# Performance work log

Measured on AMD Instinct MI355X. Metric: run time of the kernel, lower is better.

The kernel has to match this reference:

```python
import jax, jax.numpy as jnp
import numpy as np


def setup_inputs() -> dict:
    key = jax.random.key(0)
    kq, kk, kv = jax.random.split(key, 3)
    B, H, L, D = 1, 16, 4096, 64
    q = jax.random.normal(kq, (B, H, L, D), dtype=jnp.float32)
    k = jax.random.normal(kk, (B, H, L, D), dtype=jnp.float32)
    v = jax.random.normal(kv, (B, H, L, D), dtype=jnp.float32)
    return {"q": q, "k": k, "v": v}


def reference(q, k, v):
    # scale = sqrt(head_dim), matching q.size(-1) ** 0.5 in the torch module
    scale = jnp.asarray(q.shape[-1], q.dtype) ** 0.5
    # [b,h,l,m] attention scores, materialized as in the original (no flash tiling)
    attn = jnp.einsum('bhlk,bhmk->bhlm', q, k) / scale
    attn = jax.nn.softmax(attn, axis=-1)
    out = jnp.einsum('bhlm,bhmk->bhlk', attn, v)
    return out
```

## Files before the change

kernel.cpp:

```cpp
#include <hip/hip_runtime.h>
#include <hip/hip_bf16.h>


#define LSEQ 4096
#define DH   64
#define NH   16
#define QBLK 256
#define KBLK 64
#define NT   (LSEQ / KBLK)

typedef float  f32x4   __attribute__((ext_vector_type(4)));
typedef short  short8v __attribute__((ext_vector_type(8)));

__device__ __forceinline__ short f2bf(float f) {
    unsigned int u = __builtin_bit_cast(unsigned int, f);
    u = (u + 0x7FFFu + ((u >> 16) & 1u)) >> 16;
    return (short)u;
}

__device__ __forceinline__ short f2bf_rz(float f) {
    return (short)(__builtin_bit_cast(unsigned int, f) >> 16);
}

__device__ __forceinline__ short8v pack8(const float4& a, const float4& b) {
    short8v f;
    f[0] = f2bf(a.x); f[1] = f2bf(a.y); f[2] = f2bf(a.z); f[3] = f2bf(a.w);
    f[4] = f2bf(b.x); f[5] = f2bf(b.y); f[6] = f2bf(b.z); f[7] = f2bf(b.w);
    return f;
}

#define SWZ(row, slot) ((((slot) ^ ((row) & 7)) << 3))

template <int NSPLIT>
__global__ __launch_bounds__(512, 2)
void attn_fwd(const float* __restrict__ q, const float* __restrict__ k,
              const float* __restrict__ v, float* __restrict__ out,
              float* __restrict__ opart, float* __restrict__ lpart) {
    __shared__ __align__(16) short Klds[2][KBLK][64];
    __shared__ __align__(16) short Vtlds[2][DH][64];
    __shared__ __align__(16) short Plds[8][32][64];

    const int t    = threadIdx.x;
    const int w    = t >> 6;
    const int lane = t & 63;
    const int g    = lane >> 4;
    const int c    = lane & 15;
    const int h     = blockIdx.y;
    const int qtile = blockIdx.x;
    const int z     = blockIdx.z;
    constexpr int nts = NT / NSPLIT;
    const int kt0   = z * nts;

    const float* qg = q + ((size_t)h * LSEQ + (size_t)qtile * QBLK) * DH;
    const float* kg = k + (size_t)h * LSEQ * DH;
    const float* vg = v + (size_t)h * LSEQ * DH;

    const int krow  = t >> 3;
    const int kslot = t & 7;
    const int vd    = t & 63;
    const int vs    = t >> 6;

    short8v qf[2][2];
    #pragma unroll
    for (int f = 0; f < 2; ++f) {
        const int qrow = w * 32 + f * 16 + c;
        #pragma unroll
        for (int h2 = 0; h2 < 2; ++h2) {
            const float* p = &qg[(size_t)qrow * DH + h2 * 32 + g * 8];
            float4 a = *(const float4*)p;
            float4 b = *(const float4*)(p + 4);
            short8v fr;
            fr[0] = f2bf(a.x * 0.125f); fr[1] = f2bf(a.y * 0.125f);
            fr[2] = f2bf(a.z * 0.125f); fr[3] = f2bf(a.w * 0.125f);
            fr[4] = f2bf(b.x * 0.125f); fr[5] = f2bf(b.y * 0.125f);
            fr[6] = f2bf(b.z * 0.125f); fr[7] = f2bf(b.w * 0.125f);
            qf[f][h2] = fr;
        }
    }

    f32x4 o[2][4];
    #pragma unroll
    for (int f = 0; f < 2; ++f)
        #pragma unroll
        for (int i = 0; i < 4; ++i) o[f][i] = (f32x4){0.f, 0.f, 0.f, 0.f};
    float lp[2][4] = {{0.f,0.f,0.f,0.f},{0.f,0.f,0.f,0.f}};

    float4 kreg[2];
    float  vreg[8];

    {
        const int keyP = kt0 * KBLK;
        const float* p = &kg[(size_t)(keyP + krow) * DH + kslot * 8];
        kreg[0] = *(const float4*)p;
        kreg[1] = *(const float4*)(p + 4);
        #pragma unroll
        for (int j = 0; j < 8; ++j)
            vreg[j] = vg[(size_t)(keyP + vs * 8 + j) * DH + vd];
        *(short8v*)&Klds[0][krow][SWZ(krow, kslot)] = pack8(kreg[0], kreg[1]);
        short8v f8;
        #pragma unroll
        for (int j = 0; j < 8; ++j) f8[j] = f2bf_rz(vreg[j]);
        *(short8v*)&Vtlds[0][vd][SWZ(vd, vs)] = f8;
    }
    if (nts > 1) {
        const int key1 = (kt0 + 1) * KBLK;
        const float* p = &kg[(size_t)(key1 + krow) * DH + kslot * 8];
        kreg[0] = *(const float4*)p;
        kreg[1] = *(const float4*)(p + 4);
        #pragma unroll
        for (int j = 0; j < 8; ++j)
            vreg[j] = vg[(size_t)(key1 + vs * 8 + j) * DH + vd];
    }
    __syncthreads();

    short* Pw = &Plds[w][0][0];

    for (int it = 0; it < nts; ++it) {
        const int cur = it & 1;
        const int nxt = cur ^ 1;

        if (it + 1 < nts) {
            *(short8v*)&Klds[nxt][krow][SWZ(krow, kslot)] = pack8(kreg[0], kreg[1]);
            short8v f8;
            #pragma unroll
            for (int j = 0; j < 8; ++j) f8[j] = f2bf_rz(vreg[j]);
            *(short8v*)&Vtlds[nxt][vd][SWZ(vd, vs)] = f8;
        }
        if (it + 2 < nts) {
            const int key2 = (kt0 + it + 2) * KBLK;
            const float* p = &kg[(size_t)(key2 + krow) * DH + kslot * 8];
            kreg[0] = *(const float4*)p;
            kreg[1] = *(const float4*)(p + 4);
            #pragma unroll
            for (int j = 0; j < 8; ++j)
                vreg[j] = vg[(size_t)(key2 + vs * 8 + j) * DH + vd];
        }

        f32x4 sf[2][4];
        #pragma unroll
        for (int kb = 0; kb < 4; ++kb) {
            const int kr = kb * 16 + c;
            const int sw = c & 7;
            short8v k0 = *(const short8v*)&Klds[cur][kr][(g       ^ sw) << 3];
            short8v k1 = *(const short8v*)&Klds[cur][kr][((4 + g) ^ sw) << 3];
            __builtin_amdgcn_s_setprio(1);
            #pragma unroll
            for (int f = 0; f < 2; ++f) {
                f32x4 acc = (f32x4){0.f, 0.f, 0.f, 0.f};
                acc = __builtin_amdgcn_mfma_f32_16x16x32_bf16(qf[f][0], k0, acc, 0, 0, 0);
                acc = __builtin_amdgcn_mfma_f32_16x16x32_bf16(qf[f][1], k1, acc, 0, 0, 0);
                sf[f][kb] = acc;
            }
            __builtin_amdgcn_s_setprio(0);
        }

        #pragma unroll
        for (int f = 0; f < 2; ++f) {
            #pragma unroll
            for (int kb = 0; kb < 4; ++kb) {
                #pragma unroll
                for (int r = 0; r < 4; ++r) {
                    float pv = __expf(sf[f][kb][r]);
                    lp[f][r] += pv;
                    const int row = f * 16 + 4 * g + r;
                    const int col = kb * 16 + c;
                    Pw[row * 64 + SWZ(row, col >> 3) + (col & 7)] = f2bf_rz(pv);
                }
            }
        }

        #pragma unroll
        for (int kt2 = 0; kt2 < 2; ++kt2) {
            const int slot = kt2 * 4 + g;
            short8v pa0 = *(const short8v*)&Pw[(c)      * 64 + SWZ(c, slot)];
            short8v pa1 = *(const short8v*)&Pw[(16 + c) * 64 + SWZ(16 + c, slot)];
            __builtin_amdgcn_s_setprio(1);
            #pragma unroll
            for (int nf = 0; nf < 4; ++nf) {
                const int vrow = nf * 16 + c;
                short8v vb = *(const short8v*)&Vtlds[cur][vrow][SWZ(vrow, slot)];
                o[0][nf] = __builtin_amdgcn_mfma_f32_16x16x32_bf16(pa0, vb, o[0][nf], 0, 0, 0);
                o[1][nf] = __builtin_amdgcn_mfma_f32_16x16x32_bf16(pa1, vb, o[1][nf], 0, 0, 0);
            }
            __builtin_amdgcn_s_setprio(0);
        }

        __syncthreads();
    }

    #pragma unroll
    for (int mask = 1; mask < 16; mask <<= 1) {
        #pragma unroll
        for (int f = 0; f < 2; ++f)
            #pragma unroll
            for (int r = 0; r < 4; ++r)
                lp[f][r] += __shfl_xor(lp[f][r], mask, 64);
    }

    if (NSPLIT == 1) {
        float* og = out + ((size_t)h * LSEQ + (size_t)qtile * QBLK) * DH;
        #pragma unroll
        for (int f = 0; f < 2; ++f)
            #pragma unroll
            for (int r = 0; r < 4; ++r) {
                float inv = 1.0f / lp[f][r];
                const int qrow = w * 32 + f * 16 + 4 * g + r;
                #pragma unroll
                for (int nf = 0; nf < 4; ++nf)
                    og[(size_t)qrow * DH + nf * 16 + c] = o[f][nf][r] * inv;
            }
    } else {
        float* op = opart + ((size_t)(z * NH + h) * LSEQ + (size_t)qtile * QBLK) * DH;
        float* lprow = lpart + (size_t)(z * NH + h) * LSEQ + (size_t)qtile * QBLK;
        #pragma unroll
        for (int f = 0; f < 2; ++f)
            #pragma unroll
            for (int r = 0; r < 4; ++r) {
                const int qrow = w * 32 + f * 16 + 4 * g + r;
                #pragma unroll
                for (int nf = 0; nf < 4; ++nf)
                    op[(size_t)qrow * DH + nf * 16 + c] = o[f][nf][r];
                if (c == 0) lprow[qrow] = lp[f][r];
            }
    }
}

__global__ __launch_bounds__(256)
void reduce_split(const float* __restrict__ opart, const float* __restrict__ lpart,
                  float* __restrict__ out) {
    const size_t OSZ  = (size_t)NH * LSEQ * DH;
    const size_t LSZ  = (size_t)NH * LSEQ;
    const size_t TOT4 = OSZ / 4;
    for (size_t i4 = (size_t)blockIdx.x * blockDim.x + threadIdx.x; i4 < TOT4;
         i4 += (size_t)gridDim.x * blockDim.x) {
        const size_t i   = i4 * 4;
        const size_t row = i >> 6;
        float4 a = *(const float4*)&opart[i];
        float4 b = *(const float4*)&opart[OSZ + i];
        float inv = 1.0f / (lpart[row] + lpart[LSZ + row]);
        float4 r;
        r.x = (a.x + b.x) * inv; r.y = (a.y + b.y) * inv;
        r.z = (a.z + b.z) * inv; r.w = (a.w + b.w) * inv;
        *(float4*)&out[i] = r;
    }
}

extern "C" void kernel_launch(void* const* d_in, const int* in_sizes, int n_in,
                              void* d_out, int out_size, void* d_ws, size_t ws_size,
                              hipStream_t stream) {
    const float* q = (const float*)d_in[0];
    const float* k = (const float*)d_in[1];
    const float* v = (const float*)d_in[2];
    float* out = (float*)d_out;

    const size_t OSZ = (size_t)NH * LSEQ * DH;
    const size_t LSZ = (size_t)NH * LSEQ;
    const size_t need = (2 * OSZ + 2 * LSZ) * sizeof(float);

    if (ws_size >= need) {
        float* opart = (float*)d_ws;
        float* lpart = opart + 2 * OSZ;
        attn_fwd<2><<<dim3(LSEQ / QBLK, NH, 2), dim3(512), 0, stream>>>(q, k, v, out, opart, lpart);
        reduce_split<<<dim3(2048), dim3(256), 0, stream>>>(opart, lpart, out);
    } else {
        attn_fwd<1><<<dim3(LSEQ / QBLK, NH, 1), dim3(512), 0, stream>>>(q, k, v, out, nullptr, nullptr);
    }
}
```

Baseline: 197.5 us.

## Compute S transposed and shuffle P via ds_bpermute instead of LDS round-trip

Swaps the MFMA operand order so the score tile comes out transposed (keys along rows, queries along lanes). Each lane then owns a single query column, so the row sum needs only two cross-lane shuffles at the end. The exp'd probabilities are packed to bf16 pairs and rearranged into the PV A-operand layout with ds_bpermute, which removes the per-wave P buffer in shared memory and its scattered 2-byte stores. This trades LDS writes and reads for eight bpermutes per fragment plus selects, and frees shared memory that could raise occupancy.

Result: faster. 192.0 us (-2.8%).

```diff
diff --git a/kernel.cpp b/kernel.cpp
--- a/kernel.cpp
+++ b/kernel.cpp
@@ -11,6 +11,7 @@
 
 typedef float  f32x4   __attribute__((ext_vector_type(4)));
 typedef short  short8v __attribute__((ext_vector_type(8)));
+typedef int    int4v   __attribute__((ext_vector_type(4)));
 
 __device__ __forceinline__ short f2bf(float f) {
     unsigned int u = __builtin_bit_cast(unsigned int, f);
@@ -20,6 +21,11 @@
 
 __device__ __forceinline__ short f2bf_rz(float f) {
     return (short)(__builtin_bit_cast(unsigned int, f) >> 16);
+}
+
+__device__ __forceinline__ int pack_rz(float lo, float hi) {
+    return (int)((__builtin_bit_cast(unsigned int, lo) >> 16) |
+                 (__builtin_bit_cast(unsigned int, hi) & 0xffff0000u));
 }
 
 __device__ __forceinline__ short8v pack8(const float4& a, const float4& b) {
@@ -38,18 +44,21 @@
               float* __restrict__ opart, float* __restrict__ lpart) {
     __shared__ __align__(16) short Klds[2][KBLK][64];
     __shared__ __align__(16) short Vtlds[2][DH][64];
-    __shared__ __align__(16) short Plds[8][32][64];
 
     const int t    = threadIdx.x;
     const int w    = t >> 6;
     const int lane = t & 63;
     const int g    = lane >> 4;
     const int c    = lane & 15;
+    const bool ghi = lane >= 32;
     const int h     = blockIdx.y;
     const int qtile = blockIdx.x;
     const int z     = blockIdx.z;
     constexpr int nts = NT / NSPLIT;
     const int kt0   = z * nts;
+
+    const int addrA = (c + ((lane & 16) << 1)) << 2;
+    const int addrB = addrA + 64;
 
     const float* qg = q + ((size_t)h * LSEQ + (size_t)qtile * QBLK) * DH;
     const float* kg = k + (size_t)h * LSEQ * DH;
@@ -83,7 +92,7 @@
     for (int f = 0; f < 2; ++f)
         #pragma unroll
         for (int i = 0; i < 4; ++i) o[f][i] = (f32x4){0.f, 0.f, 0.f, 0.f};
-    float lp[2][4] = {{0.f,0.f,0.f,0.f},{0.f,0.f,0.f,0.f}};
+    float lp[2] = {0.f, 0.f};
 
     float4 kreg[2];
     float  vreg[8];
@@ -113,8 +122,6 @@
     }
     __syncthreads();
 
-    short* Pw = &Plds[w][0][0];
-
     for (int it = 0; it < nts; ++it) {
         const int cur = it & 1;
         const int nxt = cur ^ 1;
@@ -136,51 +143,64 @@
                 vreg[j] = vg[(size_t)(key2 + vs * 8 + j) * DH + vd];
         }
 
-        f32x4 sf[2][4];
-        #pragma unroll
-        for (int kb = 0; kb < 4; ++kb) {
-            const int kr = kb * 16 + c;
-            const int sw = c & 7;
-            short8v k0 = *(const short8v*)&Klds[cur][kr][(g       ^ sw) << 3];
-            short8v k1 = *(const short8v*)&Klds[cur][kr][((4 + g) ^ sw) << 3];
-            __builtin_amdgcn_s_setprio(1);
+        #pragma unroll
+        for (int kb2 = 0; kb2 < 2; ++kb2) {
+            int pk[2][2][2];
+            #pragma unroll
+            for (int H = 0; H < 2; ++H) {
+                const int kb = 2 * kb2 + H;
+                const int kr = kb * 16 + c;
+                const int sw = c & 7;
+                short8v k0 = *(const short8v*)&Klds[cur][kr][(g       ^ sw) << 3];
+                short8v k1 = *(const short8v*)&Klds[cur][kr][((4 + g) ^ sw) << 3];
+                __builtin_amdgcn_s_setprio(1);
+                f32x4 s0 = (f32x4){0.f, 0.f, 0.f, 0.f};
+                f32x4 s1 = (f32x4){0.f, 0.f, 0.f, 0.f};
+                s0 = __builtin_amdgcn_mfma_f32_16x16x32_bf16(k0, qf[0][0], s0, 0, 0, 0);
+                s0 = __builtin_amdgcn_mfma_f32_16x16x32_bf16(k1, qf[0][1], s0, 0, 0, 0);
+                s1 = __builtin_amdgcn_mfma_f32_16x16x32_bf16(k0, qf[1][0], s1, 0, 0, 0);
+                s1 = __builtin_amdgcn_mfma_f32_16x16x32_bf16(k1, qf[1][1], s1, 0, 0, 0);
+                __builtin_amdgcn_s_setprio(0);
+                #pragma unroll
+                for (int f = 0; f < 2; ++f) {
+                    const f32x4& s = f ? s1 : s0;
+                    float p0 = __expf(s[0]);
+                    float p1 = __expf(s[1]);
+                    float p2 = __expf(s[2]);
+                    float p3 = __expf(s[3]);
+                    lp[f] += (p0 + p1) + (p2 + p3);
+                    pk[f][H][0] = pack_rz(p0, p1);
+                    pk[f][H][1] = pack_rz(p2, p3);
+                }
+            }
+
+            short8v af[2];
             #pragma unroll
             for (int f = 0; f < 2; ++f) {
-                f32x4 acc = (f32x4){0.f, 0.f, 0.f, 0.f};
-                acc = __builtin_amdgcn_mfma_f32_16x16x32_bf16(qf[f][0], k0, acc, 0, 0, 0);
-                acc = __builtin_amdgcn_mfma_f32_16x16x32_bf16(qf[f][1], k1, acc, 0, 0, 0);
-                sf[f][kb] = acc;
-            }
-            __builtin_amdgcn_s_setprio(0);
-        }
-
-        #pragma unroll
-        for (int f = 0; f < 2; ++f) {
-            #pragma unroll
-            for (int kb = 0; kb < 4; ++kb) {
-                #pragma unroll
-                for (int r = 0; r < 4; ++r) {
-                    float pv = __expf(sf[f][kb][r]);
-                    lp[f][r] += pv;
-                    const int row = f * 16 + 4 * g + r;
-                    const int col = kb * 16 + c;
-                    Pw[row * 64 + SWZ(row, col >> 3) + (col & 7)] = f2bf_rz(pv);
-                }
-            }
-        }
-
-        #pragma unroll
-        for (int kt2 = 0; kt2 < 2; ++kt2) {
-            const int slot = kt2 * 4 + g;
-            short8v pa0 = *(const short8v*)&Pw[(c)      * 64 + SWZ(c, slot)];
-            short8v pa1 = *(const short8v*)&Pw[(16 + c) * 64 + SWZ(16 + c, slot)];
+                int lo0 = __builtin_amdgcn_ds_bpermute(addrA, pk[f][0][0]);
+                int hi0 = __builtin_amdgcn_ds_bpermute(addrA, pk[f][1][0]);
+                int lo1 = __builtin_amdgcn_ds_bpermute(addrA, pk[f][0][1]);
+                int hi1 = __builtin_amdgcn_ds_bpermute(addrA, pk[f][1][1]);
+                int lo2 = __builtin_amdgcn_ds_bpermute(addrB, pk[f][0][0]);
+                int hi2 = __builtin_amdgcn_ds_bpermute(addrB, pk[f][1][0]);
+                int lo3 = __builtin_amdgcn_ds_bpermute(addrB, pk[f][0][1]);
+                int hi3 = __builtin_amdgcn_ds_bpermute(addrB, pk[f][1][1]);
+                int4v a4;
+                a4[0] = ghi ? hi0 : lo0;
+                a4[1] = ghi ? hi1 : lo1;
+                a4[2] = ghi ? hi2 : lo2;
+                a4[3] = ghi ? hi3 : lo3;
+                af[f] = __builtin_bit_cast(short8v, a4);
+            }
+
+            const int slot = kb2 * 4 + g;
             __builtin_amdgcn_s_setprio(1);
             #pragma unroll
             for (int nf = 0; nf < 4; ++nf) {
                 const int vrow = nf * 16 + c;
                 short8v vb = *(const short8v*)&Vtlds[cur][vrow][SWZ(vrow, slot)];
-                o[0][nf] = __builtin_amdgcn_mfma_f32_16x16x32_bf16(pa0, vb, o[0][nf], 0, 0, 0);
-                o[1][nf] = __builtin_amdgcn_mfma_f32_16x16x32_bf16(pa1, vb, o[1][nf], 0, 0, 0);
+                o[0][nf] = __builtin_amdgcn_mfma_f32_16x16x32_bf16(af[0], vb, o[0][nf], 0, 0, 0);
+                o[1][nf] = __builtin_amdgcn_mfma_f32_16x16x32_bf16(af[1], vb, o[1][nf], 0, 0, 0);
             }
             __builtin_amdgcn_s_setprio(0);
         }
@@ -189,39 +209,41 @@
     }
 
     #pragma unroll
-    for (int mask = 1; mask < 16; mask <<= 1) {
-        #pragma unroll
-        for (int f = 0; f < 2; ++f)
-            #pragma unroll
-            for (int r = 0; r < 4; ++r)
-                lp[f][r] += __shfl_xor(lp[f][r], mask, 64);
+    for (int f = 0; f < 2; ++f) {
+        lp[f] += __shfl_xor(lp[f], 16, 64);
+        lp[f] += __shfl_xor(lp[f], 32, 64);
     }
 
     if (NSPLIT == 1) {
         float* og = out + ((size_t)h * LSEQ + (size_t)qtile * QBLK) * DH;
         #pragma unroll
-        for (int f = 0; f < 2; ++f)
+        for (int f = 0; f < 2; ++f) {
             #pragma unroll
             for (int r = 0; r < 4; ++r) {
-                float inv = 1.0f / lp[f][r];
+                int db = __builtin_amdgcn_ds_bpermute((4 * g + r) << 2,
+                                                      __builtin_bit_cast(int, lp[f]));
+                float inv = 1.0f / __builtin_bit_cast(float, db);
                 const int qrow = w * 32 + f * 16 + 4 * g + r;
                 #pragma unroll
                 for (int nf = 0; nf < 4; ++nf)
                     og[(size_t)qrow * DH + nf * 16 + c] = o[f][nf][r] * inv;
             }
+        }
     } else {
         float* op = opart + ((size_t)(z * NH + h) * LSEQ + (size_t)qtile * QBLK) * DH;
         float* lprow = lpart + (size_t)(z * NH + h) * LSEQ + (size_t)qtile * QBLK;
         #pragma unroll
-        for (int f = 0; f < 2; ++f)
+        for (int f = 0; f < 2; ++f) {
             #pragma unroll
             for (int r = 0; r < 4; ++r) {
                 const int qrow = w * 32 + f * 16 + 4 * g + r;
                 #pragma unroll
                 for (int nf = 0; nf < 4; ++nf)
                     op[(size_t)qrow * DH + nf * 16 + c] = o[f][nf][r];
-                if (c == 0) lprow[qrow] = lp[f][r];
-            }
+            }
+            if (lane < 16)
+                lprow[w * 32 + f * 16 + lane] = lp[f];
+        }
     }
 }
 
```
